# Kernel optimization log

Hardware: AMD Instinct MI355X
Metric: run time of the kernel (lower is better)

## Reference

```python
import jax, jax.numpy as jnp
import numpy as np

B, S, HID, NH, HD, RD, RATIO = 2, 4096, 2048, 16, 128, 64, 4
THETA = 10000.0


def _rope_tables(positions, rd, theta):
    # Unique per-pair frequencies: first half of the Llama cat([freqs, freqs], -1).
    half = rd // 2
    inv_freq = 1.0 / (theta ** (jnp.arange(half, dtype=jnp.float32) / half))
    ang = positions.astype(jnp.float32)[:, None] * inv_freq[None, :]  # [L, half]
    return jnp.cos(ang), jnp.sin(ang)


def _apply_partial_rope_interleaved(x, cos, sin, rd):
    # x: [B, H, L, D]; rotate last rd dims, pairs (2k, 2k+1). cos/sin: [L, rd//2]
    nope, rope = x[..., :-rd], x[..., -rd:]
    pr = rope.reshape(rope.shape[:-1] + (rd // 2, 2))
    a, b = pr[..., 0], pr[..., 1]
    c = cos[None, None]  # [1,1,L,half]
    s = sin[None, None]
    new = jnp.stack([a * c - b * s, a * s + b * c], axis=-1).reshape(rope.shape)
    return jnp.concatenate([nope, new], axis=-1)


def _pool_overlap(kv, gate, ape, ratio, hd):
    # kv/gate: [B, L, 2*hd]; ape: [ratio, 2*hd]. Softmax-gated sum-pool with
    # cross-window overlap: each window pools 2*ratio raw slots (prev window's
    # first-half features + current window's second-half features).
    b, length, feat = kv.shape
    n_w = length // ratio
    kv_w = kv.reshape(b, n_w, ratio, feat)
    gate_w = gate.reshape(b, n_w, ratio, feat) + ape

    def remap(t, fill):
        cur = t[..., hd:]                          # [b, n_w, ratio, hd]
        prev = t[:, :-1, :, :hd]                   # window N-1 first half
        pad = jnp.full((b, 1, ratio, hd), fill, t.dtype)
        prev = jnp.concatenate([pad, prev], axis=1)
        return jnp.concatenate([prev, cur], axis=2)  # [b, n_w, 2*ratio, hd]

    kv_o = remap(kv_w, 0.0)
    gate_o = remap(gate_w, -jnp.inf)
    w = jax.nn.softmax(gate_o, axis=2)
    return (kv_o * w).sum(axis=2)  # [b, n_w, hd]


def setup_inputs() -> dict:
    key = jax.random.key(0)
    ks = jax.random.split(key, 7)
    sc = lambda d: 1.0 / np.sqrt(d)
    return {
        "hidden": jax.random.normal(ks[0], (B, S, HID), jnp.float32),
        "wq": jax.random.normal(ks[1], (HID, NH * HD), jnp.float32) * sc(HID),
        "wkv": jax.random.normal(ks[2], (HID, 2 * HD), jnp.float32) * sc(HID),
        "wgate": jax.random.normal(ks[3], (HID, 2 * HD), jnp.float32) * sc(HID),
        "ape": jax.random.normal(ks[4], (RATIO, 2 * HD), jnp.float32) * 0.02,
        "sinks": jax.random.normal(ks[5], (NH,), jnp.float32) * 0.02,
        "wo": jax.random.normal(ks[6], (NH * HD, HID), jnp.float32) * sc(NH * HD),
        "ratio": RATIO,
        "head_dim": HD,
        "rope_head_dim": RD,
        "num_heads": NH,
    }


def reference(hidden, wq, wkv, wgate, ape, sinks, wo, ratio, head_dim, rope_head_dim, num_heads):
    b, s, _ = hidden.shape
    scale = head_dim ** -0.5

    # Projections
    q = (hidden @ wq).reshape(b, s, num_heads, head_dim).transpose(0, 2, 1, 3)  # [b,h,s,d]
    kv = hidden @ wkv      # [b, s, 2*d]
    gate = hidden @ wgate  # [b, s, 2*d]

    # Overlap gated pooling -> compressed shared KV  [b, n_w, d]
    pooled = _pool_overlap(kv, gate, ape, ratio, head_dim)
    n_w = pooled.shape[1]

    # Partial interleaved RoPE; pooled positions = w * ratio (pool_base = 0)
    q_pos = jnp.arange(s)
    k_pos = jnp.arange(n_w) * ratio
    cq, sq = _rope_tables(q_pos, rope_head_dim, THETA)
    ck, sk = _rope_tables(k_pos, rope_head_dim, THETA)
    q_rot = _apply_partial_rope_interleaved(q, cq, sq, rope_head_dim)
    k_rot = _apply_partial_rope_interleaved(pooled[:, None], ck, sk, rope_head_dim)[:, 0]  # [b,n_w,d]
    v = pooled  # [b, n_w, d]

    # Causal mask over compressed windows: query t sees window w iff its last
    # raw token (w+1)*ratio - 1 <= t.
    mask = jnp.where(q_pos[:, None] >= k_pos[None, :] + ratio - 1, 0.0, -jnp.inf)  # [s, n_w]

    scores = jnp.einsum("bhqd,bkd->bhqk", q_rot, k_rot) * scale + mask[None, None]
    sink_col = jnp.broadcast_to(sinks.reshape(1, num_heads, 1, 1), (b, num_heads, s, 1))
    combined = jnp.concatenate([scores, sink_col], axis=-1)
    probs = jax.nn.softmax(combined - jax.lax.stop_gradient(combined.max(axis=-1, keepdims=True)), axis=-1)[..., :-1]

    attn = jnp.einsum("bhqk,bkd->bhqd", probs, v)               # [b,h,s,d]
    out = attn.transpose(0, 2, 1, 3).reshape(b, s, num_heads * head_dim) @ wo
    return out
```

## Files before the change

### kernel.cpp

```cpp
#include <hip/hip_runtime.h>
#include <math.h>

typedef unsigned short u16;
typedef unsigned int   u32;
typedef __bf16 bf16x8 __attribute__((ext_vector_type(8)));
typedef float  f32x4  __attribute__((ext_vector_type(4)));

#define S_LEN 4096
#define HID   2048
#define NHEAD 16
#define HD    128
#define NW    1024
#define TOK   8192
#define LN10000 9.2103403719761836f
#define NEG_BIG (-1e30f)

__device__ __forceinline__ float b2f(u16 u){
  union { u32 i; float f; } v; v.i = ((u32)u) << 16; return v.f;
}
__device__ __forceinline__ u16 f2b(float f){
  union { float f; u32 i; } v; v.f = f;
  return (u16)((v.i + 0x7FFFu + ((v.i >> 16) & 1u)) >> 16);
}

__global__ __launch_bounds__(256) void cvt_bf16(const float* __restrict__ in,
                                                u16* __restrict__ out){
  size_t i = (size_t)blockIdx.x*256 + threadIdx.x;
  float4 a = ((const float4*)in)[2*i];
  float4 b = ((const float4*)in)[2*i+1];
  u16 t[8];
  t[0]=f2b(a.x); t[1]=f2b(a.y); t[2]=f2b(a.z); t[3]=f2b(a.w);
  t[4]=f2b(b.x); t[5]=f2b(b.y); t[6]=f2b(b.z); t[7]=f2b(b.w);
  *(uint4*)&out[i*8] = *(uint4*)t;
}

__global__ __launch_bounds__(256) void transpose_w(const float* __restrict__ in,
    u16* __restrict__ out, int K, int N){
  __shared__ float t[32][33];
  const int n0 = blockIdx.x*32, k0 = blockIdx.y*32;
  const int c = threadIdx.x & 31, r8 = threadIdx.x >> 5;
  #pragma unroll
  for (int i = 0; i < 4; i++)
    t[r8 + i*8][c] = in[(size_t)(k0 + r8 + i*8)*N + n0 + c];
  __syncthreads();
  #pragma unroll
  for (int i = 0; i < 4; i++)
    out[(size_t)(n0 + r8 + i*8)*K + k0 + c] = f2b(t[c][r8 + i*8]);
}

typedef __attribute__((address_space(3))) u16 as3_u16;
typedef __attribute__((address_space(1))) const u16 as1_u16;
__device__ __forceinline__ void gload16(const u16* g, u16* l){
  __builtin_amdgcn_global_load_lds((as1_u16*)g, (as3_u16*)l, 16, 0, 0);
}

template<typename TC>
__global__ __launch_bounds__(256) void gemm_bf16(const u16* __restrict__ A,
    const u16* __restrict__ Bt, TC* __restrict__ C, int M, int N, int K)
{
  __shared__ u16 As[128*32];
  __shared__ u16 Bs[128*32];
  const int tid  = threadIdx.x;
  const int bM   = blockIdx.y * 128;
  const int bN   = blockIdx.x * 128;
  const int lane = tid & 63;
  const int w    = tid >> 6;
  const int wm   = w >> 1, wn = w & 1;
  const int lrow = lane & 15, quad = lane >> 4;
  const int srow = lane >> 2, skc = (lane & 3) * 8;

  const u16* Ab = &A [(size_t)(bM + w*32 + srow)*K + skc];
  const u16* Bb = &Bt[(size_t)(bN + w*32 + srow)*K + skc];
  const size_t row16 = (size_t)16 * K;

  f32x4 acc[4][4];
  #pragma unroll
  for (int i = 0; i < 4; i++)
    #pragma unroll
    for (int j = 0; j < 4; j++)
      #pragma unroll
      for (int r = 0; r < 4; r++) acc[i][j][r] = 0.f;

  for (int k0 = 0; k0 < K; k0 += 32){
    gload16(Ab + k0,         &As[(w*32     )*32]);
    gload16(Ab + k0 + row16, &As[(w*32 + 16)*32]);
    gload16(Bb + k0,         &Bs[(w*32     )*32]);
    gload16(Bb + k0 + row16, &Bs[(w*32 + 16)*32]);
    __syncthreads();

    bf16x8 af[4], bfv[4];
    #pragma unroll
    for (int mf = 0; mf < 4; mf++)
      af[mf] = *(const bf16x8*)&As[(wm*64 + mf*16 + lrow)*32 + quad*8];
    #pragma unroll
    for (int nf = 0; nf < 4; nf++)
      bfv[nf] = *(const bf16x8*)&Bs[(wn*64 + nf*16 + lrow)*32 + quad*8];
    #pragma unroll
    for (int mf = 0; mf < 4; mf++)
      #pragma unroll
      for (int nf = 0; nf < 4; nf++)
        acc[mf][nf] = __builtin_amdgcn_mfma_f32_16x16x32_bf16(af[mf], bfv[nf], acc[mf][nf], 0, 0, 0);
    __syncthreads();
  }
  #pragma unroll
  for (int mf = 0; mf < 4; mf++){
    #pragma unroll
    for (int nf = 0; nf < 4; nf++){
      int gcol = bN + wn*64 + nf*16 + lrow;
      #pragma unroll
      for (int r = 0; r < 4; r++){
        int grow = bM + wm*64 + mf*16 + quad*4 + r;
        size_t idx = (size_t)grow*N + gcol;
        if constexpr (sizeof(TC) == 4) C[idx] = acc[mf][nf][r];
        else                           C[idx] = f2b(acc[mf][nf][r]);
      }
    }
  }
}

template<typename TA, typename TC>
__global__ __launch_bounds__(256) void gemm_any(const TA* __restrict__ A,
    const float* __restrict__ Bw, TC* __restrict__ C, int M, int N, int K)
{
  __shared__ u16 As[128*40];
  __shared__ u16 Bs[128*40];
  const int tid  = threadIdx.x;
  const int bM   = blockIdx.y * 128;
  const int bN   = blockIdx.x * 128;
  const int lane = tid & 63;
  const int wid  = tid >> 6;
  const int wm   = wid >> 1, wn = wid & 1;
  const int lrow = lane & 15, quad = lane >> 4;

  f32x4 acc[4][4];
  #pragma unroll
  for (int i = 0; i < 4; i++)
    #pragma unroll
    for (int j = 0; j < 4; j++)
      #pragma unroll
      for (int r = 0; r < 4; r++) acc[i][j][r] = 0.f;

  for (int k0 = 0; k0 < K; k0 += 32){
    #pragma unroll
    for (int i = 0; i < 4; i++){
      int c = tid + i*256;
      int row = c >> 3, kc = (c & 7) * 4;
      u16 tmp[4];
      if constexpr (sizeof(TA) == 4){
        float4 v = *(const float4*)&A[(size_t)(bM + row)*K + k0 + kc];
        tmp[0] = f2b(v.x); tmp[1] = f2b(v.y); tmp[2] = f2b(v.z); tmp[3] = f2b(v.w);
      } else {
        *(uint2*)tmp = *(const uint2*)&A[(size_t)(bM + row)*K + k0 + kc];
      }
      *(uint2*)&As[row*40 + kc] = *(uint2*)tmp;
    }
    #pragma unroll
    for (int i = 0; i < 4; i++){
      int c = tid + i*256;
      int kr = c >> 5, nc = (c & 31) * 4;
      float4 v = *(const float4*)&Bw[(size_t)(k0 + kr)*N + bN + nc];
      Bs[(nc+0)*40 + kr] = f2b(v.x);
      Bs[(nc+1)*40 + kr] = f2b(v.y);
      Bs[(nc+2)*40 + kr] = f2b(v.z);
      Bs[(nc+3)*40 + kr] = f2b(v.w);
    }
    __syncthreads();
    bf16x8 af[4], bfv[4];
    #pragma unroll
    for (int mf = 0; mf < 4; mf++)
      af[mf] = *(const bf16x8*)&As[(wm*64 + mf*16 + lrow)*40 + quad*8];
    #pragma unroll
    for (int nf = 0; nf < 4; nf++)
      bfv[nf] = *(const bf16x8*)&Bs[(wn*64 + nf*16 + lrow)*40 + quad*8];
    #pragma unroll
    for (int mf = 0; mf < 4; mf++)
      #pragma unroll
      for (int nf = 0; nf < 4; nf++)
        acc[mf][nf] = __builtin_amdgcn_mfma_f32_16x16x32_bf16(af[mf], bfv[nf], acc[mf][nf], 0, 0, 0);
    __syncthreads();
  }
  #pragma unroll
  for (int mf = 0; mf < 4; mf++){
    #pragma unroll
    for (int nf = 0; nf < 4; nf++){
      int gcol = bN + wn*64 + nf*16 + lrow;
      #pragma unroll
      for (int r = 0; r < 4; r++){
        int grow = bM + wm*64 + mf*16 + quad*4 + r;
        size_t idx = (size_t)grow*N + gcol;
        if constexpr (sizeof(TC) == 4) C[idx] = acc[mf][nf][r];
        else                           C[idx] = f2b(acc[mf][nf][r]);
      }
    }
  }
}

__global__ void rope_q_kernel(u16* __restrict__ q){
  int gid = blockIdx.x * 256 + threadIdx.x;
  int t = gid >> 9;
  int r = gid & 511;
  int h = r >> 5;
  int i = r & 31;
  int pos = t & (S_LEN - 1);
  float freq = expf(-(float)i * (LN10000 / 32.f));
  float ang = (float)pos * freq;
  float sn, cs;
  sincosf(ang, &sn, &cs);
  size_t off = (size_t)t*HID + h*HD + 64 + 2*i;
  float a  = b2f(q[off]);
  float bb = b2f(q[off+1]);
  q[off]   = f2b(a*cs - bb*sn);
  q[off+1] = f2b(a*sn + bb*cs);
}

__global__ void pool_rope_k(const u16* __restrict__ kv, const u16* __restrict__ gate,
                            const float* __restrict__ ape, u16* __restrict__ krot,
                            u16* __restrict__ vout, int str){
  const int d = threadIdx.x;
  const int w = blockIdx.x;
  const int b = blockIdx.y;
  __shared__ float sh[HD];
  const bool hasprev = (w > 0);
  float gc[4], vc[4], gp[4], vp[4];
  float m = NEG_BIG;
  #pragma unroll
  for (int r = 0; r < 4; r++){
    size_t t = (size_t)(b*S_LEN + w*4 + r)*str;
    vc[r] = b2f(kv[t + 128 + d]);
    gc[r] = b2f(gate[t + 128 + d]) + ape[r*256 + 128 + d];
    m = fmaxf(m, gc[r]);
  }
  if (hasprev){
    #pragma unroll
    for (int r = 0; r < 4; r++){
      size_t t = (size_t)(b*S_LEN + (w-1)*4 + r)*str;
      vp[r] = b2f(kv[t + d]);
      gp[r] = b2f(gate[t + d]) + ape[r*256 + d];
      m = fmaxf(m, gp[r]);
    }
  }
  float s = 0.f, acc = 0.f;
  #pragma unroll
  for (int r = 0; r < 4; r++){
    float e = __expf(gc[r] - m); s += e; acc += e*vc[r];
  }
  if (hasprev){
    #pragma unroll
    for (int r = 0; r < 4; r++){
      float e = __expf(gp[r] - m); s += e; acc += e*vp[r];
    }
  }
  float pooled = acc / s;
  sh[d] = pooled;
  __syncthreads();
  float kr = pooled;
  if (d >= 64){
    int i = (d - 64) >> 1;
    float freq = expf(-(float)i * (LN10000 / 32.f));
    float ang = (float)(4*w) * freq;
    float sn, cs;
    sincosf(ang, &sn, &cs);
    if ((d & 1) == 0) kr = sh[d]*cs - sh[d+1]*sn;
    else              kr = sh[d-1]*sn + sh[d]*cs;
  }
  size_t o = (size_t)(b*NW + w)*HD + d;
  krot[o] = f2b(kr);
  vout[o] = f2b(pooled);
}

#define AQT 64
#define AKT 64
#define AKSTR 136
#define AVSTR 72
#define APSTR 72
#define ATT_SCALE 0.088388347648318447f

__global__ __launch_bounds__(256, 3) void attn_kernel(
    const u16* __restrict__ qbuf, const u16* __restrict__ krot,
    const u16* __restrict__ vbuf, const float* __restrict__ sinks,
    u16* __restrict__ attnbuf)
{
  __shared__ u16 Ks[AKT*AKSTR];
  __shared__ u16 Vt[HD*AVSTR];
  __shared__ u16 Pq[AQT*APSTR];

  const int tid  = threadIdx.x;
  const int q0   = blockIdx.x * AQT;
  const int h    = blockIdx.y;
  const int b    = blockIdx.z;
  const int lane = tid & 63;
  const int wq   = tid >> 6;
  const int lrw  = lane & 15;
  const int quad = lane >> 4;
  const int qg   = q0 + wq*16 + lrw;

  bf16x8 qf[4];
  {
    const u16* qrow = &qbuf[(size_t)(b*S_LEN + qg)*HID + h*HD];
    #pragma unroll
    for (int d0 = 0; d0 < 4; d0++)
      qf[d0] = *(const bf16x8*)&qrow[d0*32 + quad*8];
  }

  float m_run = NEG_BIG, l_run = 0.f;
  f32x4 accO[8];
  #pragma unroll
  for (int ds = 0; ds < 8; ds++)
    #pragma unroll
    for (int r = 0; r < 4; r++) accO[ds][r] = 0.f;

  const int kmax_tile = (q0 + AQT - 1 - 3) >> 2;
  int nchunk = (kmax_tile >> 6) + 1;
  if (nchunk > NW/AKT) nchunk = NW/AKT;

  for (int ch = 0; ch < nchunk; ch++){
    const int kc0 = ch * AKT;
    #pragma unroll
    for (int i = 0; i < 4; i++){
      int c = tid + i*256;
      int kl = c >> 4, cc = c & 15;
      *(uint4*)&Ks[kl*AKSTR + cc*8] =
        *(const uint4*)&krot[(size_t)(b*NW + kc0 + kl)*HD + cc*8];
    }
    {
      int kl = tid & 63;
      int dbase = (tid >> 6) * 8;
      #pragma unroll
      for (int i = 0; i < 4; i++){
        int d0 = dbase + i*32;
        u16 tmp[8];
        *(uint4*)tmp = *(const uint4*)&vbuf[(size_t)(b*NW + kc0 + kl)*HD + d0];
        #pragma unroll
        for (int j = 0; j < 8; j++) Vt[(d0+j)*AVSTR + kl] = tmp[j];
      }
    }
    __syncthreads();

    f32x4 accS[4];
    #pragma unroll
    for (int ks = 0; ks < 4; ks++)
      #pragma unroll
      for (int r = 0; r < 4; r++) accS[ks][r] = 0.f;
    #pragma unroll
    for (int d0 = 0; d0 < 4; d0++){
      #pragma unroll
      for (int ks = 0; ks < 4; ks++){
        bf16x8 af = *(const bf16x8*)&Ks[(ks*16 + lrw)*AKSTR + d0*32 + quad*8];
        accS[ks] = __builtin_amdgcn_mfma_f32_16x16x32_bf16(af, qf[d0], accS[ks], 0, 0, 0);
      }
    }

    float p[16];
    float lmax = NEG_BIG;
    #pragma unroll
    for (int ks = 0; ks < 4; ks++)
      #pragma unroll
      for (int r = 0; r < 4; r++){
        int kg = kc0 + ks*16 + quad*4 + r;
        float s = (qg >= 4*kg + 3) ? accS[ks][r]*ATT_SCALE : NEG_BIG;
        p[ks*4 + r] = s;
        lmax = fmaxf(lmax, s);
      }
    lmax = fmaxf(lmax, __shfl_xor(lmax, 16));
    lmax = fmaxf(lmax, __shfl_xor(lmax, 32));
    float mnew  = fmaxf(m_run, lmax);
    float alpha = __expf(m_run - mnew);
    m_run = mnew;
    float ls = 0.f;
    #pragma unroll
    for (int i = 0; i < 16; i++){
      float e = __expf(p[i] - mnew);
      p[i] = e; ls += e;
    }
    ls += __shfl_xor(ls, 16);
    ls += __shfl_xor(ls, 32);
    l_run = l_run*alpha + ls;

    #pragma unroll
    for (int ks = 0; ks < 4; ks++){
      u16 pb[4];
      #pragma unroll
      for (int r = 0; r < 4; r++) pb[r] = f2b(p[ks*4 + r]);
      *(uint2*)&Pq[(wq*16 + lrw)*APSTR + ks*16 + quad*4] = *(uint2*)pb;
    }

    #pragma unroll
    for (int ds = 0; ds < 8; ds++)
      #pragma unroll
      for (int r = 0; r < 4; r++) accO[ds][r] *= alpha;

    #pragma unroll
    for (int kks = 0; kks < 2; kks++){
      bf16x8 pf = *(const bf16x8*)&Pq[(wq*16 + lrw)*APSTR + kks*32 + quad*8];
      #pragma unroll
      for (int ds = 0; ds < 8; ds++){
        bf16x8 av = *(const bf16x8*)&Vt[(ds*16 + lrw)*AVSTR + kks*32 + quad*8];
        accO[ds] = __builtin_amdgcn_mfma_f32_16x16x32_bf16(av, pf, accO[ds], 0, 0, 0);
      }
    }
    __syncthreads();
  }

  const float snk = sinks[h];
  float mf = fmaxf(m_run, snk);
  float em = __expf(m_run - mf);
  float sc = em / (l_run*em + __expf(snk - mf));
  size_t o = (size_t)(b*S_LEN + qg)*HID + h*HD;
  #pragma unroll
  for (int ds = 0; ds < 8; ds++){
    u16 ob[4];
    #pragma unroll
    for (int r = 0; r < 4; r++) ob[r] = f2b(accO[ds][r] * sc);
    *(uint2*)&attnbuf[o + ds*16 + quad*4] = *(uint2*)ob;
  }
}

extern "C" void kernel_launch(void* const* d_in, const int* in_sizes, int n_in,
                              void* d_out, int out_size, void* d_ws, size_t ws_size,
                              hipStream_t stream)
{
  const float* hidden = (const float*)d_in[0];
  const float* wq     = (const float*)d_in[1];
  const float* wkv    = (const float*)d_in[2];
  const float* wgate  = (const float*)d_in[3];
  const float* ape    = (const float*)d_in[4];
  const float* sinks  = (const float*)d_in[5];
  const float* wo     = (const float*)d_in[6];

  const size_t NEED = ((size_t)TOK*HID*2 + (size_t)TOK*512 + (size_t)4*NW*HD
                     + (size_t)HID*HID + (size_t)512*HID) * sizeof(u16);

  if (ws_size >= NEED){
    u16* hid_bf = (u16*)d_ws;
    u16* qbuf   = hid_bf + (size_t)TOK*HID;
    u16* kvg    = qbuf   + (size_t)TOK*HID;
    u16* krot   = kvg    + (size_t)TOK*512;
    u16* vbuf   = krot   + (size_t)2*NW*HD;
    u16* wqT    = vbuf   + (size_t)2*NW*HD;
    u16* wkvgT  = wqT    + (size_t)HID*HID;
    u16* attnbuf = hid_bf;
    u16* woT     = kvg;

    cvt_bf16<<<(TOK*HID/8)/256, 256, 0, stream>>>(hidden, hid_bf);
    transpose_w<<<dim3(HID/32, HID/32), 256, 0, stream>>>(wq, wqT, HID, HID);
    transpose_w<<<dim3(256/32, HID/32), 256, 0, stream>>>(wkv,   wkvgT,            HID, 256);
    transpose_w<<<dim3(256/32, HID/32), 256, 0, stream>>>(wgate, wkvgT + (size_t)256*HID, HID, 256);
    gemm_bf16<u16><<<dim3(HID/128, TOK/128), 256, 0, stream>>>(hid_bf, wqT,   qbuf, TOK, HID, HID);
    gemm_bf16<u16><<<dim3(512/128, TOK/128), 256, 0, stream>>>(hid_bf, wkvgT, kvg,  TOK, 512, HID);
    rope_q_kernel<<<(TOK*NHEAD*32)/256, 256, 0, stream>>>(qbuf);
    pool_rope_k<<<dim3(NW, 2), 128, 0, stream>>>(kvg, kvg + 256, ape, krot, vbuf, 512);
    attn_kernel<<<dim3(S_LEN/AQT, NHEAD, 2), 256, 0, stream>>>(qbuf, krot, vbuf, sinks, attnbuf);
    transpose_w<<<dim3(HID/32, HID/32), 256, 0, stream>>>(wo, woT, HID, HID);
    gemm_bf16<float><<<dim3(HID/128, TOK/128), 256, 0, stream>>>(attnbuf, woT, (float*)d_out, TOK, HID, HID);
  } else {
    u16* qbuf    = (u16*)d_ws;
    u16* kvbuf   = qbuf    + (size_t)TOK*HID;
    u16* gatebuf = kvbuf   + (size_t)TOK*256;
    u16* krot    = gatebuf + (size_t)TOK*256;
    u16* vbuf    = krot    + (size_t)2*NW*HD;
    u16* attnbuf = vbuf    + (size_t)2*NW*HD;

    gemm_any<float,u16><<<dim3(HID/128, TOK/128), 256, 0, stream>>>(hidden, wq,    qbuf,    TOK, HID, HID);
    gemm_any<float,u16><<<dim3(256/128, TOK/128), 256, 0, stream>>>(hidden, wkv,   kvbuf,   TOK, 256, HID);
    gemm_any<float,u16><<<dim3(256/128, TOK/128), 256, 0, stream>>>(hidden, wgate, gatebuf, TOK, 256, HID);
    rope_q_kernel<<<(TOK*NHEAD*32)/256, 256, 0, stream>>>(qbuf);
    pool_rope_k<<<dim3(NW, 2), 128, 0, stream>>>(kvbuf, gatebuf, ape, krot, vbuf, 256);
    attn_kernel<<<dim3(S_LEN/AQT, NHEAD, 2), 256, 0, stream>>>(qbuf, krot, vbuf, sinks, attnbuf);
    gemm_any<u16,float><<<dim3(HID/128, TOK/128), 256, 0, stream>>>(attnbuf, wo, (float*)d_out, TOK, HID, HID);
  }
}
```

Baseline: 557.4 us.

## Enlarge attention query tile, pre-transpose V in pooling, reverse block order

The attention kernel now gives each wave two 16-row query groups, so each block covers 128 queries. Every K and V tile loaded into shared memory is reused by twice as many MFMAs, and K/V global traffic drops. The pooling kernel writes V already transposed, which replaces the strided scalar shared-memory transpose in the inner loop with vectorized copies. Blocks are launched in reverse query order so the long causal tiles start first, at the cost of more registers and occupancy lowered to 2 blocks per CU.

```diff
diff --git a/kernel.cpp b/kernel.cpp
--- a/kernel.cpp
+++ b/kernel.cpp
@@ -215,7 +215,7 @@
 
 __global__ void pool_rope_k(const u16* __restrict__ kv, const u16* __restrict__ gate,
                             const float* __restrict__ ape, u16* __restrict__ krot,
-                            u16* __restrict__ vout, int str){
+                            u16* __restrict__ vT, int str){
   const int d = threadIdx.x;
   const int w = blockIdx.x;
   const int b = blockIdx.y;
@@ -263,21 +263,20 @@
     if ((d & 1) == 0) kr = sh[d]*cs - sh[d+1]*sn;
     else              kr = sh[d-1]*sn + sh[d]*cs;
   }
-  size_t o = (size_t)(b*NW + w)*HD + d;
-  krot[o] = f2b(kr);
-  vout[o] = f2b(pooled);
-}
-
-#define AQT 64
+  krot[(size_t)(b*NW + w)*HD + d] = f2b(kr);
+  vT[(size_t)(b*HD + d)*NW + w]   = f2b(pooled);
+}
+
+#define AQT 128
 #define AKT 64
 #define AKSTR 136
 #define AVSTR 72
 #define APSTR 72
 #define ATT_SCALE 0.088388347648318447f
 
-__global__ __launch_bounds__(256, 3) void attn_kernel(
+__global__ __launch_bounds__(256, 2) void attn_kernel(
     const u16* __restrict__ qbuf, const u16* __restrict__ krot,
-    const u16* __restrict__ vbuf, const float* __restrict__ sinks,
+    const u16* __restrict__ vT, const float* __restrict__ sinks,
     u16* __restrict__ attnbuf)
 {
   __shared__ u16 Ks[AKT*AKSTR];
@@ -285,29 +284,33 @@
   __shared__ u16 Pq[AQT*APSTR];
 
   const int tid  = threadIdx.x;
-  const int q0   = blockIdx.x * AQT;
+  const int q0   = (int)(gridDim.x - 1 - blockIdx.x) * AQT;
   const int h    = blockIdx.y;
   const int b    = blockIdx.z;
   const int lane = tid & 63;
   const int wq   = tid >> 6;
   const int lrw  = lane & 15;
   const int quad = lane >> 4;
-  const int qg   = q0 + wq*16 + lrw;
-
-  bf16x8 qf[4];
-  {
-    const u16* qrow = &qbuf[(size_t)(b*S_LEN + qg)*HID + h*HD];
+  const int qg0  = q0 + wq*32 + lrw;
+
+  bf16x8 qf[2][4];
+  #pragma unroll
+  for (int g = 0; g < 2; g++){
+    const u16* qrow = &qbuf[(size_t)(b*S_LEN + qg0 + g*16)*HID + h*HD];
     #pragma unroll
     for (int d0 = 0; d0 < 4; d0++)
-      qf[d0] = *(const bf16x8*)&qrow[d0*32 + quad*8];
-  }
-
-  float m_run = NEG_BIG, l_run = 0.f;
-  f32x4 accO[8];
-  #pragma unroll
-  for (int ds = 0; ds < 8; ds++)
-    #pragma unroll
-    for (int r = 0; r < 4; r++) accO[ds][r] = 0.f;
+      qf[g][d0] = *(const bf16x8*)&qrow[d0*32 + quad*8];
+  }
+
+  float m_run[2] = {NEG_BIG, NEG_BIG};
+  float l_run[2] = {0.f, 0.f};
+  f32x4 accO[2][8];
+  #pragma unroll
+  for (int g = 0; g < 2; g++)
+    #pragma unroll
+    for (int ds = 0; ds < 8; ds++)
+      #pragma unroll
+      for (int r = 0; r < 4; r++) accO[g][ds][r] = 0.f;
 
   const int kmax_tile = (q0 + AQT - 1 - 3) >> 2;
   int nchunk = (kmax_tile >> 6) + 1;
@@ -318,100 +321,109 @@
     #pragma unroll
     for (int i = 0; i < 4; i++){
       int c = tid + i*256;
-      int kl = c >> 4, cc = c & 15;
-      *(uint4*)&Ks[kl*AKSTR + cc*8] =
-        *(const uint4*)&krot[(size_t)(b*NW + kc0 + kl)*HD + cc*8];
-    }
-    {
-      int kl = tid & 63;
-      int dbase = (tid >> 6) * 8;
-      #pragma unroll
-      for (int i = 0; i < 4; i++){
-        int d0 = dbase + i*32;
-        u16 tmp[8];
-        *(uint4*)tmp = *(const uint4*)&vbuf[(size_t)(b*NW + kc0 + kl)*HD + d0];
+      int kl = c >> 4, cc = (c & 15) * 8;
+      *(uint4*)&Ks[kl*AKSTR + cc] =
+        *(const uint4*)&krot[(size_t)(b*NW + kc0 + kl)*HD + cc];
+    }
+    #pragma unroll
+    for (int i = 0; i < 4; i++){
+      int c = tid + i*256;
+      int dv = c >> 3, cc = (c & 7) * 8;
+      *(uint4*)&Vt[dv*AVSTR + cc] =
+        *(const uint4*)&vT[(size_t)(b*HD + dv)*NW + kc0 + cc];
+    }
+    __syncthreads();
+
+    f32x4 accS[2][4];
+    #pragma unroll
+    for (int g = 0; g < 2; g++)
+      #pragma unroll
+      for (int ks = 0; ks < 4; ks++)
         #pragma unroll
-        for (int j = 0; j < 8; j++) Vt[(d0+j)*AVSTR + kl] = tmp[j];
-      }
-    }
-    __syncthreads();
-
-    f32x4 accS[4];
-    #pragma unroll
-    for (int ks = 0; ks < 4; ks++)
-      #pragma unroll
-      for (int r = 0; r < 4; r++) accS[ks][r] = 0.f;
+        for (int r = 0; r < 4; r++) accS[g][ks][r] = 0.f;
     #pragma unroll
     for (int d0 = 0; d0 < 4; d0++){
       #pragma unroll
       for (int ks = 0; ks < 4; ks++){
-        bf16x8 af = *(const bf16x8*)&Ks[(ks*16 + lrw)*AKSTR + d0*32 + quad*8];
-        accS[ks] = __builtin_amdgcn_mfma_f32_16x16x32_bf16(af, qf[d0], accS[ks], 0, 0, 0);
-      }
-    }
-
-    float p[16];
-    float lmax = NEG_BIG;
-    #pragma unroll
-    for (int ks = 0; ks < 4; ks++)
-      #pragma unroll
-      for (int r = 0; r < 4; r++){
-        int kg = kc0 + ks*16 + quad*4 + r;
-        float s = (qg >= 4*kg + 3) ? accS[ks][r]*ATT_SCALE : NEG_BIG;
-        p[ks*4 + r] = s;
-        lmax = fmaxf(lmax, s);
-      }
-    lmax = fmaxf(lmax, __shfl_xor(lmax, 16));
-    lmax = fmaxf(lmax, __shfl_xor(lmax, 32));
-    float mnew  = fmaxf(m_run, lmax);
-    float alpha = __expf(m_run - mnew);
-    m_run = mnew;
-    float ls = 0.f;
-    #pragma unroll
-    for (int i = 0; i < 16; i++){
-      float e = __expf(p[i] - mnew);
-      p[i] = e; ls += e;
-    }
-    ls += __shfl_xor(ls, 16);
-    ls += __shfl_xor(ls, 32);
-    l_run = l_run*alpha + ls;
-
-    #pragma unroll
-    for (int ks = 0; ks < 4; ks++){
-      u16 pb[4];
-      #pragma unroll
-      for (int r = 0; r < 4; r++) pb[r] = f2b(p[ks*4 + r]);
-      *(uint2*)&Pq[(wq*16 + lrw)*APSTR + ks*16 + quad*4] = *(uint2*)pb;
-    }
-
-    #pragma unroll
-    for (int ds = 0; ds < 8; ds++)
-      #pragma unroll
-      for (int r = 0; r < 4; r++) accO[ds][r] *= alpha;
+        bf16x8 kf = *(const bf16x8*)&Ks[(ks*16 + lrw)*AKSTR + d0*32 + quad*8];
+        accS[0][ks] = __builtin_amdgcn_mfma_f32_16x16x32_bf16(kf, qf[0][d0], accS[0][ks], 0, 0, 0);
+        accS[1][ks] = __builtin_amdgcn_mfma_f32_16x16x32_bf16(kf, qf[1][d0], accS[1][ks], 0, 0, 0);
+      }
+    }
+
+    float alpha[2];
+    #pragma unroll
+    for (int g = 0; g < 2; g++){
+      const int qg = qg0 + g*16;
+      float p[16];
+      float lmax = NEG_BIG;
+      #pragma unroll
+      for (int ks = 0; ks < 4; ks++)
+        #pragma unroll
+        for (int r = 0; r < 4; r++){
+          int kg = kc0 + ks*16 + quad*4 + r;
+          float s = (qg >= 4*kg + 3) ? accS[g][ks][r]*ATT_SCALE : NEG_BIG;
+          p[ks*4 + r] = s;
+          lmax = fmaxf(lmax, s);
+        }
+      lmax = fmaxf(lmax, __shfl_xor(lmax, 16));
+      lmax = fmaxf(lmax, __shfl_xor(lmax, 32));
+      float mnew = fmaxf(m_run[g], lmax);
+      alpha[g] = __expf(m_run[g] - mnew);
+      m_run[g] = mnew;
+      float ls = 0.f;
+      #pragma unroll
+      for (int i = 0; i < 16; i++){
+        float e = __expf(p[i] - mnew);
+        p[i] = e; ls += e;
+      }
+      ls += __shfl_xor(ls, 16);
+      ls += __shfl_xor(ls, 32);
+      l_run[g] = l_run[g]*alpha[g] + ls;
+      #pragma unroll
+      for (int ks = 0; ks < 4; ks++){
+        u16 pb[4];
+        #pragma unroll
+        for (int r = 0; r < 4; r++) pb[r] = f2b(p[ks*4 + r]);
+        *(uint2*)&Pq[(wq*32 + g*16 + lrw)*APSTR + ks*16 + quad*4] = *(uint2*)pb;
+      }
+    }
+
+    #pragma unroll
+    for (int g = 0; g < 2; g++)
+      #pragma unroll
+      for (int ds = 0; ds < 8; ds++)
+        #pragma unroll
+        for (int r = 0; r < 4; r++) accO[g][ds][r] *= alpha[g];
 
     #pragma unroll
     for (int kks = 0; kks < 2; kks++){
-      bf16x8 pf = *(const bf16x8*)&Pq[(wq*16 + lrw)*APSTR + kks*32 + quad*8];
+      bf16x8 pf0 = *(const bf16x8*)&Pq[(wq*32      + lrw)*APSTR + kks*32 + quad*8];
+      bf16x8 pf1 = *(const bf16x8*)&Pq[(wq*32 + 16 + lrw)*APSTR + kks*32 + quad*8];
       #pragma unroll
       for (int ds = 0; ds < 8; ds++){
         bf16x8 av = *(const bf16x8*)&Vt[(ds*16 + lrw)*AVSTR + kks*32 + quad*8];
-        accO[ds] = __builtin_amdgcn_mfma_f32_16x16x32_bf16(av, pf, accO[ds], 0, 0, 0);
+        accO[0][ds] = __builtin_amdgcn_mfma_f32_16x16x32_bf16(av, pf0, accO[0][ds], 0, 0, 0);
+        accO[1][ds] = __builtin_amdgcn_mfma_f32_16x16x32_bf16(av, pf1, accO[1][ds], 0, 0, 0);
       }
     }
     __syncthreads();
   }
 
   const float snk = sinks[h];
-  float mf = fmaxf(m_run, snk);
-  float em = __expf(m_run - mf);
-  float sc = em / (l_run*em + __expf(snk - mf));
-  size_t o = (size_t)(b*S_LEN + qg)*HID + h*HD;
-  #pragma unroll
-  for (int ds = 0; ds < 8; ds++){
-    u16 ob[4];
-    #pragma unroll
-    for (int r = 0; r < 4; r++) ob[r] = f2b(accO[ds][r] * sc);
-    *(uint2*)&attnbuf[o + ds*16 + quad*4] = *(uint2*)ob;
+  #pragma unroll
+  for (int g = 0; g < 2; g++){
+    float mf = fmaxf(m_run[g], snk);
+    float em = __expf(m_run[g] - mf);
+    float sc = em / (l_run[g]*em + __expf(snk - mf));
+    size_t o = (size_t)(b*S_LEN + qg0 + g*16)*HID + h*HD;
+    #pragma unroll
+    for (int ds = 0; ds < 8; ds++){
+      u16 ob[4];
+      #pragma unroll
+      for (int r = 0; r < 4; r++) ob[r] = f2b(accO[g][ds][r] * sc);
+      *(uint2*)&attnbuf[o + ds*16 + quad*4] = *(uint2*)ob;
+    }
   }
 }
 
@@ -435,8 +447,8 @@
     u16* qbuf   = hid_bf + (size_t)TOK*HID;
     u16* kvg    = qbuf   + (size_t)TOK*HID;
     u16* krot   = kvg    + (size_t)TOK*512;
-    u16* vbuf   = krot   + (size_t)2*NW*HD;
-    u16* wqT    = vbuf   + (size_t)2*NW*HD;
+    u16* vTb    = krot   + (size_t)2*NW*HD;
+    u16* wqT    = vTb    + (size_t)2*NW*HD;
     u16* wkvgT  = wqT    + (size_t)HID*HID;
     u16* attnbuf = hid_bf;
     u16* woT     = kvg;
@@ -448,8 +460,8 @@
     gemm_bf16<u16><<<dim3(HID/128, TOK/128), 256, 0, stream>>>(hid_bf, wqT,   qbuf, TOK, HID, HID);
     gemm_bf16<u16><<<dim3(512/128, TOK/128), 256, 0, stream>>>(hid_bf, wkvgT, kvg,  TOK, 512, HID);
     rope_q_kernel<<<(TOK*NHEAD*32)/256, 256, 0, stream>>>(qbuf);
-    pool_rope_k<<<dim3(NW, 2), 128, 0, stream>>>(kvg, kvg + 256, ape, krot, vbuf, 512);
-    attn_kernel<<<dim3(S_LEN/AQT, NHEAD, 2), 256, 0, stream>>>(qbuf, krot, vbuf, sinks, attnbuf);
+    pool_rope_k<<<dim3(NW, 2), 128, 0, stream>>>(kvg, kvg + 256, ape, krot, vTb, 512);
+    attn_kernel<<<dim3(S_LEN/AQT, NHEAD, 2), 256, 0, stream>>>(qbuf, krot, vTb, sinks, attnbuf);
     transpose_w<<<dim3(HID/32, HID/32), 256, 0, stream>>>(wo, woT, HID, HID);
     gemm_bf16<float><<<dim3(HID/128, TOK/128), 256, 0, stream>>>(attnbuf, woT, (float*)d_out, TOK, HID, HID);
   } else {
@@ -457,15 +469,15 @@
     u16* kvbuf   = qbuf    + (size_t)TOK*HID;
     u16* gatebuf = kvbuf   + (size_t)TOK*256;
     u16* krot    = gatebuf + (size_t)TOK*256;
-    u16* vbuf    = krot    + (size_t)2*NW*HD;
-    u16* attnbuf = vbuf    + (size_t)2*NW*HD;
+    u16* vTb     = krot    + (size_t)2*NW*HD;
+    u16* attnbuf = vTb     + (size_t)2*NW*HD;
 
     gemm_any<float,u16><<<dim3(HID/128, TOK/128), 256, 0, stream>>>(hidden, wq,    qbuf,    TOK, HID, HID);
     gemm_any<float,u16><<<dim3(256/128, TOK/128), 256, 0, stream>>>(hidden, wkv,   kvbuf,   TOK, 256, HID);
     gemm_any<float,u16><<<dim3(256/128, TOK/128), 256, 0, stream>>>(hidden, wgate, gatebuf, TOK, 256, HID);
     rope_q_kernel<<<(TOK*NHEAD*32)/256, 256, 0, stream>>>(qbuf);
-    pool_rope_k<<<dim3(NW, 2), 128, 0, stream>>>(kvbuf, gatebuf, ape, krot, vbuf, 256);
-    attn_kernel<<<dim3(S_LEN/AQT, NHEAD, 2), 256, 0, stream>>>(qbuf, krot, vbuf, sinks, attnbuf);
+    pool_rope_k<<<dim3(NW, 2), 128, 0, stream>>>(kvbuf, gatebuf, ape, krot, vTb, 256);
+    attn_kernel<<<dim3(S_LEN/AQT, NHEAD, 2), 256, 0, stream>>>(qbuf, krot, vTb, sinks, attnbuf);
     gemm_any<u16,float><<<dim3(HID/128, TOK/128), 256, 0, stream>>>(attnbuf, wo, (float*)d_out, TOK, HID, HID);
   }
 }
```

New measurement: 546.4 us. 2.0% less time.
